# Optimization experiments

Hardware: AMD Instinct MI355X
Metric: run time of the kernel (lower is better)

Reference implementation:

```python
import jax, jax.numpy as jnp
import numpy as np

H = 1024
B = 64
S = 1024
V = 50257
L = 3  # GRU layers


def setup_inputs() -> dict:
    key = jax.random.key(0)
    ks = jax.random.split(key, 12)
    sc = 0.02
    return {
        "input_seq": jax.random.randint(ks[0], (B,), 0, V),
        "last_hidden": jax.random.normal(ks[1], (L, B, H), jnp.float32) * sc,
        "encoder_outputs": jax.random.normal(ks[2], (S, B, H), jnp.float32) * sc,
        "emb_table": jax.random.normal(ks[3], (V, H), jnp.float32) * sc,
        "w_ih": jax.random.normal(ks[4], (L, 3 * H, H), jnp.float32) * sc,
        "w_hh": jax.random.normal(ks[5], (L, 3 * H, H), jnp.float32) * sc,
        "b_ih": jax.random.normal(ks[6], (L, 3 * H), jnp.float32) * sc,
        "b_hh": jax.random.normal(ks[7], (L, 3 * H), jnp.float32) * sc,
        "concat_w": jax.random.normal(ks[8], (H, 2 * H), jnp.float32) * sc,
        "concat_b": jax.random.normal(ks[9], (H,), jnp.float32) * sc,
        "out_w": jax.random.normal(ks[10], (V, H), jnp.float32) * sc,
        "out_b": jax.random.normal(ks[11], (V,), jnp.float32) * sc,
    }


def _gru_step(x, h, w_ih, w_hh, b_ih, b_hh):
    # x, h: [B, H]; weights per PyTorch GRU layout (r, z, n gates stacked)
    gi = x @ w_ih.T + b_ih  # [B, 3H]
    gh = h @ w_hh.T + b_hh  # [B, 3H]
    i_r, i_z, i_n = jnp.split(gi, 3, axis=-1)
    h_r, h_z, h_n = jnp.split(gh, 3, axis=-1)
    r = jax.nn.sigmoid(i_r + h_r)
    z = jax.nn.sigmoid(i_z + h_z)
    n = jnp.tanh(i_n + r * h_n)
    return (1.0 - z) * n + z * h


def reference(input_seq, last_hidden, encoder_outputs, emb_table,
              w_ih, w_hh, b_ih, b_hh, concat_w, concat_b, out_w, out_b):
    # Embed current token (decoder uses its own embedding of size hidden_dim).
    x = emb_table[input_seq]  # [B, H]; dropout is identity at eval time
    # 3-layer GRU, single time step.
    new_h = []
    for l in range(L):
        h_l = _gru_step(x, last_hidden[l], w_ih[l], w_hh[l], b_ih[l], b_hh[l])
        new_h.append(h_l)
        x = h_l  # inter-layer dropout is identity at eval time
    hidden = jnp.stack(new_h, axis=0)  # [L, B, H]
    rnn_output = x  # [B, H] (top layer output, seq len 1)
    # Dot attention: score(b, s) = <rnn_output[b], encoder_outputs[s, b]>
    scores = jnp.einsum('bh,sbh->bs', rnn_output, encoder_outputs)  # [B, S]
    attn = jax.nn.softmax(scores, axis=-1)  # [B, S]
    attn_weights = attn[:, None, :]  # [B, 1, S]
    context = jnp.einsum('bs,sbh->bh', attn, encoder_outputs)  # [B, H]
    concat_input = jnp.concatenate([rnn_output, context], axis=-1)  # [B, 2H]
    concat_output = jnp.tanh(concat_input @ concat_w.T + concat_b)  # [B, H]
    output = concat_output @ out_w.T + out_b  # [B, V]
    return (output, hidden, attn_weights)
```

## Files before the change

### kernel.cpp

```cpp
#include <hip/hip_runtime.h>
#include <hip/hip_bf16.h>
#include <float.h>

#define B_ 64
#define H_ 1024
#define S_ 1024
#define V_ 50257
#define L_ 3
#define G3H 3072
#define N_GATES 6144
#define NT_K 16

typedef __attribute__((ext_vector_type(8))) short short8v;
typedef __attribute__((ext_vector_type(4))) float f32x4;

__device__ __forceinline__ ushort rnd_bf16(float x) {
    uint u = __float_as_uint(x);
    return (ushort)((u + 0x7fffu + ((u >> 16) & 1u)) >> 16);
}

__device__ __forceinline__ void split_bf16(float x, ushort& hi, ushort& lo) {
    uint u = __float_as_uint(x);
    uint h = u & 0xffff0000u;
    hi = (ushort)(h >> 16);
    float r = x - __uint_as_float(h);
    uint ur = __float_as_uint(r);
    lo = (ushort)((ur + 0x7fffu + ((ur >> 16) & 1u)) >> 16);
}

__device__ __forceinline__ int swzi(int kk, int m) {
    return (((m >> 2) ^ ((kk >> 2) & 7)) << 2) | (m & 3);
}

__global__ __launch_bounds__(256) void embed_k(const int* __restrict__ seq,
                                               const float* __restrict__ emb,
                                               float* __restrict__ x0) {
    int idx = blockIdx.x * 256 + threadIdx.x;
    int b = idx >> 10, h = idx & 1023;
    x0[idx] = emb[(size_t)seq[b] * H_ + h];
}

__global__ __launch_bounds__(256) void gemm_m64(
    const float* __restrict__ A0, const float* __restrict__ A1, int lda,
    const float* __restrict__ W0, const float* __restrict__ W1, int ldw,
    int Nhalf, float* __restrict__ Cpart, int N, int K) {
    __shared__ float As[32 * 68];
    __shared__ float Ws[32 * 68];

    int n0 = blockIdx.x * 64;
    const float* A = A0;
    const float* W = W0;
    int ncol0 = n0;
    if (n0 >= Nhalf) { A = A1; W = W1; ncol0 = n0 - Nhalf; }

    int tid = threadIdx.x;
    int tx = tid & 15, ty = tid >> 4;
    int row = tid >> 3;
    int cg = tid & 7;

    float acc[4][4] = {};

    int kChunk = K / gridDim.y;
    int k0b = blockIdx.y * kChunk;

    for (int k0 = k0b; k0 < k0b + kChunk; k0 += 32) {
        float4 a0 = *(const float4*)&A[(size_t)row * lda + k0 + cg * 4];
        float4 a1 = *(const float4*)&A[(size_t)(row + 32) * lda + k0 + cg * 4];
        float4 w0 = *(const float4*)&W[(size_t)(ncol0 + row) * ldw + k0 + cg * 4];
        float4 w1 = *(const float4*)&W[(size_t)(ncol0 + row + 32) * ldw + k0 + cg * 4];
        const float* fa0 = (const float*)&a0;
        const float* fa1 = (const float*)&a1;
        const float* fw0 = (const float*)&w0;
        const float* fw1 = (const float*)&w1;
#pragma unroll
        for (int j = 0; j < 4; j++) {
            int kk = cg * 4 + j;
            As[kk * 68 + swzi(kk, row)] = fa0[j];
            As[kk * 68 + swzi(kk, row + 32)] = fa1[j];
            Ws[kk * 68 + swzi(kk, row)] = fw0[j];
            Ws[kk * 68 + swzi(kk, row + 32)] = fw1[j];
        }
        __syncthreads();
#pragma unroll
        for (int kk = 0; kk < 32; kk++) {
            int cgk = (kk >> 2) & 7;
            float4 av = *(const float4*)&As[kk * 68 + ((ty ^ cgk) << 2)];
            float4 wv = *(const float4*)&Ws[kk * 68 + ((tx ^ cgk) << 2)];
            acc[0][0] += av.x * wv.x; acc[0][1] += av.x * wv.y;
            acc[0][2] += av.x * wv.z; acc[0][3] += av.x * wv.w;
            acc[1][0] += av.y * wv.x; acc[1][1] += av.y * wv.y;
            acc[1][2] += av.y * wv.z; acc[1][3] += av.y * wv.w;
            acc[2][0] += av.z * wv.x; acc[2][1] += av.z * wv.y;
            acc[2][2] += av.z * wv.z; acc[2][3] += av.z * wv.w;
            acc[3][0] += av.w * wv.x; acc[3][1] += av.w * wv.y;
            acc[3][2] += av.w * wv.z; acc[3][3] += av.w * wv.w;
        }
        __syncthreads();
    }

    float* P = Cpart + (size_t)blockIdx.y * 64 * N;
#pragma unroll
    for (int i = 0; i < 4; i++) {
        int m = ty * 4 + i;
#pragma unroll
        for (int j = 0; j < 4; j++) {
            int n = n0 + tx * 4 + j;
            P[(size_t)m * N + n] = acc[i][j];
        }
    }
}

__global__ __launch_bounds__(256) void gru_combine_k(
    const float* __restrict__ P, const float* __restrict__ b_ih,
    const float* __restrict__ b_hh, const float* __restrict__ hprev,
    float* __restrict__ hout) {
    int idx = blockIdx.x * 256 + threadIdx.x;
    int b = idx >> 10, j = idx & 1023;
    const size_t stride = (size_t)64 * N_GATES;
    const float* rowp = P + (size_t)b * N_GATES;

    float ir = 0.f, iz = 0.f, in_ = 0.f, hr = 0.f, hz = 0.f, hn = 0.f;
#pragma unroll
    for (int kc = 0; kc < 4; kc++) {
        const float* p = rowp + kc * stride;
        ir += p[j];        iz += p[j + 1024];        in_ += p[j + 2048];
        hr += p[3072 + j]; hz += p[3072 + j + 1024]; hn += p[3072 + j + 2048];
    }
    ir += b_ih[j]; iz += b_ih[j + 1024]; in_ += b_ih[j + 2048];
    hr += b_hh[j]; hz += b_hh[j + 1024]; hn += b_hh[j + 2048];

    float r = 1.f / (1.f + __expf(-(ir + hr)));
    float z = 1.f / (1.f + __expf(-(iz + hz)));
    float n = tanhf(in_ + r * hn);
    float hp = hprev[idx];
    hout[idx] = (1.f - z) * n + z * hp;
}

__global__ __launch_bounds__(256) void attn_pass1(
    const float* __restrict__ rnn, const float* __restrict__ enc,
    float* __restrict__ scores, float* __restrict__ ctxPart,
    float* __restrict__ chunkMax) {
    __shared__ float lm[4];
    __shared__ float lc[4][1024];

    int bid = blockIdx.x;
    int b = bid >> 4, scv = bid & 15;
    int tid = threadIdx.x;
    int w = tid >> 6, lane = tid & 63;

    const float4* rr = (const float4*)(rnn + (size_t)b * H_);
    float4 r0 = rr[0 * 64 + lane], r1 = rr[1 * 64 + lane];
    float4 r2 = rr[2 * 64 + lane], r3 = rr[3 * 64 + lane];

    float m = -FLT_MAX;
    float4 c0 = {0, 0, 0, 0}, c1 = {0, 0, 0, 0}, c2 = {0, 0, 0, 0}, c3 = {0, 0, 0, 0};

    int s0 = scv * 64 + w * 16;
    for (int si = 0; si < 16; si++) {
        int s = s0 + si;
        const float4* er = (const float4*)(enc + ((size_t)s * B_ + b) * H_);
        float4 e0 = er[0 * 64 + lane], e1 = er[1 * 64 + lane];
        float4 e2 = er[2 * 64 + lane], e3 = er[3 * 64 + lane];

        float d = e0.x * r0.x + e0.y * r0.y + e0.z * r0.z + e0.w * r0.w;
        d += e1.x * r1.x + e1.y * r1.y + e1.z * r1.z + e1.w * r1.w;
        d += e2.x * r2.x + e2.y * r2.y + e2.z * r2.z + e2.w * r2.w;
        d += e3.x * r3.x + e3.y * r3.y + e3.z * r3.z + e3.w * r3.w;
#pragma unroll
        for (int off = 32; off; off >>= 1) d += __shfl_xor(d, off, 64);
        if (lane == 0) scores[(size_t)b * S_ + s] = d;

        if (d > m) {
            float scale = __expf(m - d);
            c0.x *= scale; c0.y *= scale; c0.z *= scale; c0.w *= scale;
            c1.x *= scale; c1.y *= scale; c1.z *= scale; c1.w *= scale;
            c2.x *= scale; c2.y *= scale; c2.z *= scale; c2.w *= scale;
            c3.x *= scale; c3.y *= scale; c3.z *= scale; c3.w *= scale;
            m = d;
        }
        float p = __expf(d - m);
        c0.x += p * e0.x; c0.y += p * e0.y; c0.z += p * e0.z; c0.w += p * e0.w;
        c1.x += p * e1.x; c1.y += p * e1.y; c1.z += p * e1.z; c1.w += p * e1.w;
        c2.x += p * e2.x; c2.y += p * e2.y; c2.z += p * e2.z; c2.w += p * e2.w;
        c3.x += p * e3.x; c3.y += p * e3.y; c3.z += p * e3.z; c3.w += p * e3.w;
    }

    if (lane == 0) lm[w] = m;
    __syncthreads();
    float M = fmaxf(fmaxf(lm[0], lm[1]), fmaxf(lm[2], lm[3]));
    float sw = __expf(m - M);
    float4* lw = (float4*)&lc[w][0];
    float4 t;
    t.x = c0.x * sw; t.y = c0.y * sw; t.z = c0.z * sw; t.w = c0.w * sw; lw[0 * 64 + lane] = t;
    t.x = c1.x * sw; t.y = c1.y * sw; t.z = c1.z * sw; t.w = c1.w * sw; lw[1 * 64 + lane] = t;
    t.x = c2.x * sw; t.y = c2.y * sw; t.z = c2.z * sw; t.w = c2.w * sw; lw[2 * 64 + lane] = t;
    t.x = c3.x * sw; t.y = c3.y * sw; t.z = c3.z * sw; t.w = c3.w * sw; lw[3 * 64 + lane] = t;
    __syncthreads();

    float4 s4 = *(const float4*)&lc[0][tid * 4];
    float4 a1 = *(const float4*)&lc[1][tid * 4];
    float4 a2 = *(const float4*)&lc[2][tid * 4];
    float4 a3 = *(const float4*)&lc[3][tid * 4];
    s4.x += a1.x + a2.x + a3.x; s4.y += a1.y + a2.y + a3.y;
    s4.z += a1.z + a2.z + a3.z; s4.w += a1.w + a2.w + a3.w;
    *(float4*)&ctxPart[(size_t)bid * H_ + tid * 4] = s4;
    if (tid == 0) chunkMax[bid] = M;
}

__global__ __launch_bounds__(256) void attn_pass2(
    const float* __restrict__ scores, const float* __restrict__ chunkMax,
    const float* __restrict__ ctxPart, const float* __restrict__ rnn,
    float* __restrict__ attn, float* __restrict__ concat_in) {
    __shared__ float red[256];
    int b = blockIdx.x, tid = threadIdx.x;

    float v[4];
#pragma unroll
    for (int q = 0; q < 4; q++) v[q] = scores[(size_t)b * S_ + q * 256 + tid];
    float mx = fmaxf(fmaxf(v[0], v[1]), fmaxf(v[2], v[3]));
    red[tid] = mx; __syncthreads();
    for (int s = 128; s; s >>= 1) {
        if (tid < s) red[tid] = fmaxf(red[tid], red[tid + s]);
        __syncthreads();
    }
    float M = red[0]; __syncthreads();
    float e[4], sum = 0.f;
#pragma unroll
    for (int q = 0; q < 4; q++) { e[q] = __expf(v[q] - M); sum += e[q]; }
    red[tid] = sum; __syncthreads();
    for (int s = 128; s; s >>= 1) {
        if (tid < s) red[tid] += red[tid + s];
        __syncthreads();
    }
    float inv = 1.f / red[0];
#pragma unroll
    for (int q = 0; q < 4; q++) attn[(size_t)b * S_ + q * 256 + tid] = e[q] * inv;

    float4 acc = {0, 0, 0, 0};
#pragma unroll
    for (int c = 0; c < 16; c++) {
        float scl = __expf(chunkMax[b * 16 + c] - M);
        float4 part = *(const float4*)&ctxPart[((size_t)b * 16 + c) * H_ + tid * 4];
        acc.x += scl * part.x; acc.y += scl * part.y;
        acc.z += scl * part.z; acc.w += scl * part.w;
    }
    acc.x *= inv; acc.y *= inv; acc.z *= inv; acc.w *= inv;
    *(float4*)&concat_in[(size_t)b * 2048 + 1024 + tid * 4] = acc;
    *(float4*)&concat_in[(size_t)b * 2048 + tid * 4] =
        *(const float4*)&rnn[(size_t)b * H_ + tid * 4];
}

__global__ __launch_bounds__(256) void concat_combine_k(const float* __restrict__ P,
                                                        const float* __restrict__ bias,
                                                        ushort* __restrict__ Ahi,
                                                        ushort* __restrict__ Alo) {
    int idx = blockIdx.x * 256 + threadIdx.x;
    int b = idx >> 10, h = idx & 1023;
    float s = 0.f;
#pragma unroll
    for (int kc = 0; kc < 8; kc++) s += P[(size_t)kc * 65536 + (size_t)b * H_ + h];
    float v = tanhf(s + bias[h]);
    ushort hi, lo;
    split_bf16(v, hi, lo);
    Ahi[idx] = hi;
    Alo[idx] = lo;
}

__global__ __launch_bounds__(256) void gemm_out_bf16(
    const ushort* __restrict__ Ahi, const ushort* __restrict__ Alo,
    const float* __restrict__ W, const float* __restrict__ bias,
    float* __restrict__ out) {
    __shared__ ushort AhL[2][64 * 64];
    __shared__ ushort AlL[2][64 * 64];
    __shared__ ushort WtL[2][64 * 64];

    int tid = threadIdx.x;
    int w = tid >> 6, l = tid & 63;
    int lr = l & 15;
    int lk = l >> 4;

    int n0 = blockIdx.x * 64;

    int srow = tid >> 2;
    int sq = tid & 3;
    int wrow_g = n0 + srow;
    const float* Wsrc = W + (size_t)(wrow_g < V_ ? wrow_g : 0) * H_;

    union SV { short8v v; ushort u[8]; };

    short8v rAh0, rAh1, rAl0, rAl1;
    float4 rW[4];

    auto load_regs = [&](int kt) {
        int kb = kt * 64 + sq * 16;
        rAh0 = *(const short8v*)&Ahi[(size_t)srow * H_ + kb];
        rAh1 = *(const short8v*)&Ahi[(size_t)srow * H_ + kb + 8];
        rAl0 = *(const short8v*)&Alo[(size_t)srow * H_ + kb];
        rAl1 = *(const short8v*)&Alo[(size_t)srow * H_ + kb + 8];
#pragma unroll
        for (int i = 0; i < 4; i++) rW[i] = *(const float4*)&Wsrc[kb + i * 4];
    };

    auto write_lds = [&](int buf) {
        int s0 = (2 * sq) ^ (srow & 7);
        int s1 = (2 * sq + 1) ^ (srow & 7);
        int base = srow * 64;
        *(short8v*)&AhL[buf][base + s0 * 8] = rAh0;
        *(short8v*)&AhL[buf][base + s1 * 8] = rAh1;
        *(short8v*)&AlL[buf][base + s0 * 8] = rAl0;
        *(short8v*)&AlL[buf][base + s1 * 8] = rAl1;
        SV p0, p1;
        const float* f = (const float*)&rW[0];
#pragma unroll
        for (int j = 0; j < 8; j++) {
            p0.u[j] = rnd_bf16(f[j]);
            p1.u[j] = rnd_bf16(f[8 + j]);
        }
        *(short8v*)&WtL[buf][base + s0 * 8] = p0.v;
        *(short8v*)&WtL[buf][base + s1 * 8] = p1.v;
    };

    f32x4 acc[4];
#pragma unroll
    for (int mt = 0; mt < 4; mt++) acc[mt] = (f32x4){0.f, 0.f, 0.f, 0.f};

    load_regs(0);
    write_lds(0);
    __syncthreads();

    int wrow = w * 16 + lr;
    for (int kt = 0; kt < NT_K; kt++) {
        if (kt + 1 < NT_K) load_regs(kt + 1);

        int cur = kt & 1;
#pragma unroll
        for (int ks = 0; ks < 2; ks++) {
            int slot = ks * 4 + lk;
            short8v wf = *(const short8v*)&WtL[cur][wrow * 64 + ((slot ^ (wrow & 7)) << 3)];
#pragma unroll
            for (int mt = 0; mt < 4; mt++) {
                int arow = mt * 16 + lr;
                int so = (slot ^ (arow & 7)) << 3;
                short8v ah = *(const short8v*)&AhL[cur][arow * 64 + so];
                short8v al = *(const short8v*)&AlL[cur][arow * 64 + so];
                acc[mt] = __builtin_amdgcn_mfma_f32_16x16x32_bf16(ah, wf, acc[mt], 0, 0, 0);
                acc[mt] = __builtin_amdgcn_mfma_f32_16x16x32_bf16(al, wf, acc[mt], 0, 0, 0);
            }
        }

        if (kt + 1 < NT_K) {
            write_lds((kt + 1) & 1);
            __syncthreads();
        }
    }

    __syncthreads();
    float* et = (float*)&AhL[0][0];
#pragma unroll
    for (int mt = 0; mt < 4; mt++) {
#pragma unroll
        for (int r = 0; r < 4; r++) {
            int row = mt * 16 + lk * 4 + r;
            et[row * 64 + wrow] = acc[mt][r];
        }
    }
    __syncthreads();

    int col = tid & 63;
    int gc = n0 + col;
    int rg = tid >> 6;
    if (gc < V_) {
        float b = bias[gc];
#pragma unroll
        for (int rr = 0; rr < 16; rr++) {
            int orow = rg * 16 + rr;
            out[(size_t)orow * V_ + gc] = et[orow * 64 + col] + b;
        }
    }
}

extern "C" void kernel_launch(void* const* d_in, const int* in_sizes, int n_in,
                              void* d_out, int out_size, void* d_ws, size_t ws_size,
                              hipStream_t stream) {
    const int* seq = (const int*)d_in[0];
    const float* last_hidden = (const float*)d_in[1];
    const float* enc = (const float*)d_in[2];
    const float* emb = (const float*)d_in[3];
    const float* w_ih = (const float*)d_in[4];
    const float* w_hh = (const float*)d_in[5];
    const float* b_ih = (const float*)d_in[6];
    const float* b_hh = (const float*)d_in[7];
    const float* concat_w = (const float*)d_in[8];
    const float* concat_b = (const float*)d_in[9];
    const float* out_w = (const float*)d_in[10];
    const float* out_b = (const float*)d_in[11];

    float* out = (float*)d_out;
    float* out_hidden = out + (size_t)B_ * V_;
    float* out_attn = out_hidden + (size_t)L_ * B_ * H_;

    float* ws = (float*)d_ws;
    float* x0 = ws;
    float* gatesP = x0 + 65536;
    float* scores = gatesP + 1572864;
    float* chunkMax = scores + 65536;
    float* ctxPart = chunkMax + 1024;
    float* concat_in = ctxPart + 1048576;
    float* concatP = concat_in + 131072;
    ushort* Ahi = (ushort*)(concatP + 524288);
    ushort* Alo = Ahi + 65536;

    embed_k<<<256, 256, 0, stream>>>(seq, emb, x0);

    for (int l = 0; l < L_; l++) {
        const float* xl = (l == 0) ? x0 : out_hidden + (size_t)(l - 1) * B_ * H_;
        const float* hl = last_hidden + (size_t)l * B_ * H_;
        gemm_m64<<<dim3(N_GATES / 64, 4), 256, 0, stream>>>(
            xl, hl, H_,
            w_ih + (size_t)l * G3H * H_, w_hh + (size_t)l * G3H * H_, H_, G3H,
            gatesP, N_GATES, H_);
        gru_combine_k<<<256, 256, 0, stream>>>(gatesP, b_ih + (size_t)l * G3H,
                                               b_hh + (size_t)l * G3H, hl,
                                               out_hidden + (size_t)l * B_ * H_);
    }
    const float* rnn = out_hidden + (size_t)2 * B_ * H_;

    attn_pass1<<<1024, 256, 0, stream>>>(rnn, enc, scores, ctxPart, chunkMax);
    attn_pass2<<<64, 256, 0, stream>>>(scores, chunkMax, ctxPart, rnn,
                                       out_attn, concat_in);

    gemm_m64<<<dim3(16, 8), 256, 0, stream>>>(
        concat_in, concat_in, 2048, concat_w, concat_w, 2048, 1 << 30,
        concatP, H_, 2048);
    concat_combine_k<<<256, 256, 0, stream>>>(concatP, concat_b, Ahi, Alo);

    gemm_out_bf16<<<(V_ + 63) / 64, 256, 0, stream>>>(Ahi, Alo, out_w, out_b, out);
}
```

Baseline: 218.8 us.

## Use split-bf16 MFMA GEMM for GRU and concat layers, fuse embedding gather

Replaces the FP32 SIMT GEMM used for the GRU gate and concat projections with a double-buffered LDS GEMM on bf16 MFMA, where activations are split into hi/lo bf16 pairs and weights are rounded to bf16. The embedding lookup is folded into the first-layer GEMM through an indirect row index, which removes a separate kernel launch. K-split factors are doubled (8 for GRU, 16 for concat) so more blocks run at once, with larger partial-sum buffers to match. Rounding the weights to bf16 lowers precision compared with FP32, and the combine kernels now have to reduce more partial sums.

```diff
diff --git a/kernel.cpp b/kernel.cpp
--- a/kernel.cpp
+++ b/kernel.cpp
@@ -10,6 +10,8 @@
 #define G3H 3072
 #define N_GATES 6144
 #define NT_K 16
+#define KSPL_GRU 8
+#define KSPL_CAT 16
 
 typedef __attribute__((ext_vector_type(8))) short short8v;
 typedef __attribute__((ext_vector_type(4))) float f32x4;
@@ -28,84 +30,111 @@
     lo = (ushort)((ur + 0x7fffu + ((ur >> 16) & 1u)) >> 16);
 }
 
-__device__ __forceinline__ int swzi(int kk, int m) {
-    return (((m >> 2) ^ ((kk >> 2) & 7)) << 2) | (m & 3);
-}
-
-__global__ __launch_bounds__(256) void embed_k(const int* __restrict__ seq,
-                                               const float* __restrict__ emb,
-                                               float* __restrict__ x0) {
-    int idx = blockIdx.x * 256 + threadIdx.x;
-    int b = idx >> 10, h = idx & 1023;
-    x0[idx] = emb[(size_t)seq[b] * H_ + h];
-}
-
-__global__ __launch_bounds__(256) void gemm_m64(
-    const float* __restrict__ A0, const float* __restrict__ A1, int lda,
+__global__ __launch_bounds__(256) void gemm_bf16_lds(
+    const float* __restrict__ A0, const int* __restrict__ seq,
+    const float* __restrict__ A1, int lda,
     const float* __restrict__ W0, const float* __restrict__ W1, int ldw,
     int Nhalf, float* __restrict__ Cpart, int N, int K) {
-    __shared__ float As[32 * 68];
-    __shared__ float Ws[32 * 68];
+    __shared__ ushort AhL[2][64 * 64];
+    __shared__ ushort AlL[2][64 * 64];
+    __shared__ ushort WtL[2][64 * 64];
+
+    int tid = threadIdx.x;
+    int w = tid >> 6, l = tid & 63;
+    int lr = l & 15;
+    int lk = l >> 4;
 
     int n0 = blockIdx.x * 64;
     const float* A = A0;
     const float* W = W0;
+    const int* sq = seq;
     int ncol0 = n0;
-    if (n0 >= Nhalf) { A = A1; W = W1; ncol0 = n0 - Nhalf; }
-
-    int tid = threadIdx.x;
-    int tx = tid & 15, ty = tid >> 4;
-    int row = tid >> 3;
-    int cg = tid & 7;
-
-    float acc[4][4] = {};
+    if (n0 >= Nhalf) { A = A1; W = W1; ncol0 = n0 - Nhalf; sq = nullptr; }
+
+    int srow = tid >> 2;
+    int sqk = tid & 3;
+    const float* Asrc = A + (size_t)(sq ? sq[srow] : srow) * lda;
+    const float* Wsrc = W + (size_t)(ncol0 + srow) * ldw;
 
     int kChunk = K / gridDim.y;
-    int k0b = blockIdx.y * kChunk;
-
-    for (int k0 = k0b; k0 < k0b + kChunk; k0 += 32) {
-        float4 a0 = *(const float4*)&A[(size_t)row * lda + k0 + cg * 4];
-        float4 a1 = *(const float4*)&A[(size_t)(row + 32) * lda + k0 + cg * 4];
-        float4 w0 = *(const float4*)&W[(size_t)(ncol0 + row) * ldw + k0 + cg * 4];
-        float4 w1 = *(const float4*)&W[(size_t)(ncol0 + row + 32) * ldw + k0 + cg * 4];
-        const float* fa0 = (const float*)&a0;
-        const float* fa1 = (const float*)&a1;
-        const float* fw0 = (const float*)&w0;
-        const float* fw1 = (const float*)&w1;
-#pragma unroll
-        for (int j = 0; j < 4; j++) {
-            int kk = cg * 4 + j;
-            As[kk * 68 + swzi(kk, row)] = fa0[j];
-            As[kk * 68 + swzi(kk, row + 32)] = fa1[j];
-            Ws[kk * 68 + swzi(kk, row)] = fw0[j];
-            Ws[kk * 68 + swzi(kk, row + 32)] = fw1[j];
-        }
-        __syncthreads();
-#pragma unroll
-        for (int kk = 0; kk < 32; kk++) {
-            int cgk = (kk >> 2) & 7;
-            float4 av = *(const float4*)&As[kk * 68 + ((ty ^ cgk) << 2)];
-            float4 wv = *(const float4*)&Ws[kk * 68 + ((tx ^ cgk) << 2)];
-            acc[0][0] += av.x * wv.x; acc[0][1] += av.x * wv.y;
-            acc[0][2] += av.x * wv.z; acc[0][3] += av.x * wv.w;
-            acc[1][0] += av.y * wv.x; acc[1][1] += av.y * wv.y;
-            acc[1][2] += av.y * wv.z; acc[1][3] += av.y * wv.w;
-            acc[2][0] += av.z * wv.x; acc[2][1] += av.z * wv.y;
-            acc[2][2] += av.z * wv.z; acc[2][3] += av.z * wv.w;
-            acc[3][0] += av.w * wv.x; acc[3][1] += av.w * wv.y;
-            acc[3][2] += av.w * wv.z; acc[3][3] += av.w * wv.w;
-        }
-        __syncthreads();
-    }
-
-    float* P = Cpart + (size_t)blockIdx.y * 64 * N;
-#pragma unroll
-    for (int i = 0; i < 4; i++) {
-        int m = ty * 4 + i;
-#pragma unroll
-        for (int j = 0; j < 4; j++) {
-            int n = n0 + tx * 4 + j;
-            P[(size_t)m * N + n] = acc[i][j];
+    int kBeg = blockIdx.y * kChunk;
+    int nt = kChunk >> 6;
+
+    union SV { short8v v; ushort u[8]; };
+
+    float4 rA[4], rW[4];
+    auto load_regs = [&](int kt) {
+        int kb = kBeg + kt * 64 + sqk * 16;
+#pragma unroll
+        for (int i = 0; i < 4; i++) {
+            rA[i] = *(const float4*)&Asrc[kb + i * 4];
+            rW[i] = *(const float4*)&Wsrc[kb + i * 4];
+        }
+    };
+    auto write_lds = [&](int buf) {
+        int s0 = (2 * sqk) ^ (srow & 7);
+        int s1 = (2 * sqk + 1) ^ (srow & 7);
+        int base = srow * 64;
+        SV h0, h1, l0, l1, q0, q1;
+        const float* fa = (const float*)&rA[0];
+        const float* fw = (const float*)&rW[0];
+#pragma unroll
+        for (int j = 0; j < 8; j++) {
+            split_bf16(fa[j], h0.u[j], l0.u[j]);
+            split_bf16(fa[8 + j], h1.u[j], l1.u[j]);
+            q0.u[j] = rnd_bf16(fw[j]);
+            q1.u[j] = rnd_bf16(fw[8 + j]);
+        }
+        *(short8v*)&AhL[buf][base + s0 * 8] = h0.v;
+        *(short8v*)&AhL[buf][base + s1 * 8] = h1.v;
+        *(short8v*)&AlL[buf][base + s0 * 8] = l0.v;
+        *(short8v*)&AlL[buf][base + s1 * 8] = l1.v;
+        *(short8v*)&WtL[buf][base + s0 * 8] = q0.v;
+        *(short8v*)&WtL[buf][base + s1 * 8] = q1.v;
+    };
+
+    f32x4 acc[4];
+#pragma unroll
+    for (int mt = 0; mt < 4; mt++) acc[mt] = (f32x4){0.f, 0.f, 0.f, 0.f};
+
+    load_regs(0);
+    write_lds(0);
+    __syncthreads();
+
+    int wrow = w * 16 + lr;
+    for (int kt = 0; kt < nt; kt++) {
+        if (kt + 1 < nt) load_regs(kt + 1);
+
+        int cur = kt & 1;
+#pragma unroll
+        for (int ks = 0; ks < 2; ks++) {
+            int slot = ks * 4 + lk;
+            short8v wf = *(const short8v*)&WtL[cur][wrow * 64 + ((slot ^ (wrow & 7)) << 3)];
+#pragma unroll
+            for (int mt = 0; mt < 4; mt++) {
+                int arow = mt * 16 + lr;
+                int so = (slot ^ (arow & 7)) << 3;
+                short8v ah = *(const short8v*)&AhL[cur][arow * 64 + so];
+                short8v al = *(const short8v*)&AlL[cur][arow * 64 + so];
+                acc[mt] = __builtin_amdgcn_mfma_f32_16x16x32_bf16(ah, wf, acc[mt], 0, 0, 0);
+                acc[mt] = __builtin_amdgcn_mfma_f32_16x16x32_bf16(al, wf, acc[mt], 0, 0, 0);
+            }
+        }
+
+        if (kt + 1 < nt) {
+            write_lds((kt + 1) & 1);
+            __syncthreads();
+        }
+    }
+
+    float* Pp = Cpart + (size_t)blockIdx.y * 64 * N;
+    int col = n0 + wrow;
+#pragma unroll
+    for (int mt = 0; mt < 4; mt++) {
+#pragma unroll
+        for (int r = 0; r < 4; r++) {
+            int row = mt * 16 + lk * 4 + r;
+            Pp[(size_t)row * N + col] = acc[mt][r];
         }
     }
 }
@@ -121,7 +150,7 @@
 
     float ir = 0.f, iz = 0.f, in_ = 0.f, hr = 0.f, hz = 0.f, hn = 0.f;
 #pragma unroll
-    for (int kc = 0; kc < 4; kc++) {
+    for (int kc = 0; kc < KSPL_GRU; kc++) {
         const float* p = rowp + kc * stride;
         ir += p[j];        iz += p[j + 1024];        in_ += p[j + 2048];
         hr += p[3072 + j]; hz += p[3072 + j + 1024]; hn += p[3072 + j + 2048];
@@ -258,7 +287,7 @@
     int b = idx >> 10, h = idx & 1023;
     float s = 0.f;
 #pragma unroll
-    for (int kc = 0; kc < 8; kc++) s += P[(size_t)kc * 65536 + (size_t)b * H_ + h];
+    for (int kc = 0; kc < KSPL_CAT; kc++) s += P[(size_t)kc * 65536 + (size_t)b * H_ + h];
     float v = tanhf(s + bias[h]);
     ushort hi, lo;
     split_bf16(v, hi, lo);
@@ -282,7 +311,7 @@
     int n0 = blockIdx.x * 64;
 
     int srow = tid >> 2;
-    int sq = tid & 3;
+    int sqk = tid & 3;
     int wrow_g = n0 + srow;
     const float* Wsrc = W + (size_t)(wrow_g < V_ ? wrow_g : 0) * H_;
 
@@ -292,7 +321,7 @@
     float4 rW[4];
 
     auto load_regs = [&](int kt) {
-        int kb = kt * 64 + sq * 16;
+        int kb = kt * 64 + sqk * 16;
         rAh0 = *(const short8v*)&Ahi[(size_t)srow * H_ + kb];
         rAh1 = *(const short8v*)&Ahi[(size_t)srow * H_ + kb + 8];
         rAl0 = *(const short8v*)&Alo[(size_t)srow * H_ + kb];
@@ -302,8 +331,8 @@
     };
 
     auto write_lds = [&](int buf) {
-        int s0 = (2 * sq) ^ (srow & 7);
-        int s1 = (2 * sq + 1) ^ (srow & 7);
+        int s0 = (2 * sqk) ^ (srow & 7);
+        int s1 = (2 * sqk + 1) ^ (srow & 7);
         int base = srow * 64;
         *(short8v*)&AhL[buf][base + s0 * 8] = rAh0;
         *(short8v*)&AhL[buf][base + s1 * 8] = rAh1;
@@ -400,23 +429,21 @@
     float* out_attn = out_hidden + (size_t)L_ * B_ * H_;
 
     float* ws = (float*)d_ws;
-    float* x0 = ws;
-    float* gatesP = x0 + 65536;
-    float* scores = gatesP + 1572864;
+    float* gatesP = ws;
+    float* scores = gatesP + 3145728;
     float* chunkMax = scores + 65536;
     float* ctxPart = chunkMax + 1024;
     float* concat_in = ctxPart + 1048576;
     float* concatP = concat_in + 131072;
-    ushort* Ahi = (ushort*)(concatP + 524288);
+    ushort* Ahi = (ushort*)(concatP + 1048576);
     ushort* Alo = Ahi + 65536;
 
-    embed_k<<<256, 256, 0, stream>>>(seq, emb, x0);
-
     for (int l = 0; l < L_; l++) {
-        const float* xl = (l == 0) ? x0 : out_hidden + (size_t)(l - 1) * B_ * H_;
+        const float* xl = (l == 0) ? emb : out_hidden + (size_t)(l - 1) * B_ * H_;
+        const int* sq = (l == 0) ? seq : nullptr;
         const float* hl = last_hidden + (size_t)l * B_ * H_;
-        gemm_m64<<<dim3(N_GATES / 64, 4), 256, 0, stream>>>(
-            xl, hl, H_,
+        gemm_bf16_lds<<<dim3(N_GATES / 64, KSPL_GRU), 256, 0, stream>>>(
+            xl, sq, hl, H_,
             w_ih + (size_t)l * G3H * H_, w_hh + (size_t)l * G3H * H_, H_, G3H,
             gatesP, N_GATES, H_);
         gru_combine_k<<<256, 256, 0, stream>>>(gatesP, b_ih + (size_t)l * G3H,
@@ -429,8 +456,8 @@
     attn_pass2<<<64, 256, 0, stream>>>(scores, chunkMax, ctxPart, rnn,
                                        out_attn, concat_in);
 
-    gemm_m64<<<dim3(16, 8), 256, 0, stream>>>(
-        concat_in, concat_in, 2048, concat_w, concat_w, 2048, 1 << 30,
+    gemm_bf16_lds<<<dim3(H_ / 64, KSPL_CAT), 256, 0, stream>>>(
+        concat_in, nullptr, concat_in, 2048, concat_w, concat_w, 2048, 1 << 30,
         concatP, H_, 2048);
     concat_combine_k<<<256, 256, 0, stream>>>(concatP, concat_b, Ahi, Alo);
 
```

Measured after the change: 184.0 us, median of 2. -15.9%, faster.
